# Optimization experiments

Measured on AMD Instinct MI355X. Metric: run time of the kernel, lower is better.

Reference implementation:

```python
import jax, jax.numpy as jnp
import numpy as np

D_MODEL = 1024
NUM_HEADS = 16
HEAD_DIM = D_MODEL // NUM_HEADS
MAX_SEQ_LEN = 2048
THETA = 10000.0
BATCH = 2
SEQ = 2048


def _rope_tables():
    inv_freq = 1.0 / (THETA ** (jnp.arange(0, HEAD_DIM, 2, dtype=jnp.float32) / HEAD_DIM))
    pos = jnp.arange(MAX_SEQ_LEN, dtype=jnp.float32)
    freqs = pos[:, None] * inv_freq[None, :]  # [max_seq, head_dim/2]
    return jnp.sin(freqs), jnp.cos(freqs)


def _apply_rope(x, sin, cos):
    # x: [b, h, s, d]; sin/cos: [s, d/2] -> broadcast over b, h
    sin = sin[None, None, :, :]
    cos = cos[None, None, :, :]
    x_even = x[..., 0::2]
    x_odd = x[..., 1::2]
    out_even = x_even * cos - x_odd * sin
    out_odd = x_even * sin + x_odd * cos
    # interleave back: stack on new last axis then flatten
    out = jnp.stack((out_even, out_odd), axis=-1)
    return out.reshape(x.shape)


def setup_inputs() -> dict:
    key = jax.random.key(0)
    ks = jax.random.split(key, 5)
    std = (2.0 / (D_MODEL + D_MODEL)) ** 0.5
    return {
        "x": jax.random.normal(ks[0], (BATCH, SEQ, D_MODEL), dtype=jnp.float32),
        "Wq": jax.random.normal(ks[1], (D_MODEL, D_MODEL), dtype=jnp.float32) * std,
        "Wk": jax.random.normal(ks[2], (D_MODEL, D_MODEL), dtype=jnp.float32) * std,
        "Wv": jax.random.normal(ks[3], (D_MODEL, D_MODEL), dtype=jnp.float32) * std,
        "Wo": jax.random.normal(ks[4], (D_MODEL, D_MODEL), dtype=jnp.float32) * std,
    }


def reference(x, Wq, Wk, Wv, Wo):
    b, s, _ = x.shape
    # projections: weight stored [out, in] as in the torch Linear
    Q = jnp.einsum('bsd,od->bso', x, Wq)
    K = jnp.einsum('bsd,od->bso', x, Wk)
    V = jnp.einsum('bsd,od->bso', x, Wv)
    # split heads -> [b, h, s, hd]
    def split(t):
        return t.reshape(b, s, NUM_HEADS, HEAD_DIM).transpose(0, 2, 1, 3)
    Q, K, V = split(Q), split(K), split(V)
    sin, cos = _rope_tables()
    sin, cos = sin[:s], cos[:s]
    Q = _apply_rope(Q, sin, cos)
    K = _apply_rope(K, sin, cos)
    scale = 1.0 / jnp.sqrt(jnp.float32(HEAD_DIM))
    scores = jnp.einsum('bhqd,bhkd->bhqk', Q, K)
    causal = jnp.tril(jnp.ones((s, s), dtype=bool))[None, None]
    scores = jnp.where(causal, scores, -jnp.inf) * scale  # -inf * scale stays -inf
    attn = jax.nn.softmax(scores, axis=-1)
    out = jnp.einsum('bhqk,bhkd->bhqd', attn, V)
    out = out.transpose(0, 2, 1, 3).reshape(b, s, D_MODEL)
    return jnp.einsum('bsd,od->bso', out, Wo)
```

## Files before the change

### kernel.cpp

```cpp
#include <hip/hip_runtime.h>
#include <math.h>

#define NHEADS 16
#define HD 64
#define SEQ 2048
#define BATCH 2
#define DM 1024
#define MTOT (BATCH*SEQ)
#define LDP 72

typedef __bf16 bf16x8 __attribute__((ext_vector_type(8)));
typedef __bf16 bf16x4 __attribute__((ext_vector_type(4)));
typedef float  f32x4  __attribute__((ext_vector_type(4)));

#define LOG2E 1.4426950408889634f

#define GLD16(gp, lp) __builtin_amdgcn_global_load_lds( \
    (const __attribute__((address_space(1))) void*)(gp), \
    (__attribute__((address_space(3))) void*)(lp), 16, 0, 0)

__global__ __launch_bounds__(256)
void cast_all(const float* __restrict__ x, const float* __restrict__ Wq,
              const float* __restrict__ Wk, const float* __restrict__ Wv,
              const float* __restrict__ Wo,
              __bf16* __restrict__ xb, __bf16* __restrict__ Wqkvb,
              __bf16* __restrict__ Wob)
{
    const size_t NX = (size_t)MTOT * DM;
    const size_t NW = (size_t)DM * DM;
    const size_t i = ((size_t)blockIdx.x * 256 + threadIdx.x) * 8;
    const float* src; __bf16* dst; size_t off;
    if (i < NX)               { src = x;  dst = xb;           off = i; }
    else if (i < NX + NW)     { src = Wq; dst = Wqkvb;        off = i - NX; }
    else if (i < NX + 2*NW)   { src = Wk; dst = Wqkvb + NW;   off = i - NX - NW; }
    else if (i < NX + 3*NW)   { src = Wv; dst = Wqkvb + 2*NW; off = i - NX - 2*NW; }
    else                      { src = Wo; dst = Wob;          off = i - NX - 3*NW; }
    const float4 f0 = *(const float4*)&src[off];
    const float4 f1 = *(const float4*)&src[off + 4];
    bf16x8 o;
    o[0] = (__bf16)f0.x; o[1] = (__bf16)f0.y; o[2] = (__bf16)f0.z; o[3] = (__bf16)f0.w;
    o[4] = (__bf16)f1.x; o[5] = (__bf16)f1.y; o[6] = (__bf16)f1.z; o[7] = (__bf16)f1.w;
    *(bf16x8*)&dst[off] = o;
}

__global__ __launch_bounds__(256)
void gemm_mfma(const __bf16* __restrict__ A, const __bf16* __restrict__ W,
               float* __restrict__ Cf,
               __bf16* __restrict__ Qb, __bf16* __restrict__ Kb,
               __bf16* __restrict__ Vtb, int mode)
{
    __shared__ __bf16 As[128 * 32];
    __shared__ __bf16 Bs[128 * 32];

    const int tid  = threadIdx.x;
    const int lane = tid & 63;
    const int wave = tid >> 6;
    const int ll   = lane & 15;
    const int quad = lane >> 4;
    const int wm   = (wave & 1) * 64;
    const int wn   = (wave >> 1) * 64;
    const int bm   = blockIdx.x * 128;
    const int bn   = blockIdx.y * 128;

    const __bf16* Ab = A + (size_t)bm * DM;
    const __bf16* Wb = W + (size_t)bn * DM;

    f32x4 acc[4][4];
#pragma unroll
    for (int i = 0; i < 4; i++)
#pragma unroll
        for (int j = 0; j < 4; j++) acc[i][j] = (f32x4){0.f, 0.f, 0.f, 0.f};

    const int t0 = tid, t1 = tid + 256;
    const int ar0 = t0 >> 2, ac0 = (t0 & 3) * 8;
    const int ar1 = t1 >> 2, ac1 = (t1 & 3) * 8;

    for (int k0 = 0; k0 < DM; k0 += 32) {
        GLD16(Ab + (size_t)ar0 * DM + k0 + ac0, &As[t0 * 8]);
        GLD16(Ab + (size_t)ar1 * DM + k0 + ac1, &As[t1 * 8]);
        GLD16(Wb + (size_t)ar0 * DM + k0 + ac0, &Bs[t0 * 8]);
        GLD16(Wb + (size_t)ar1 * DM + k0 + ac1, &Bs[t1 * 8]);
        __syncthreads();

        bf16x8 af[4], bfr[4];
#pragma unroll
        for (int i = 0; i < 4; i++)
            af[i] = *(const bf16x8*)&As[(wm + i*16 + ll) * 32 + quad * 8];
#pragma unroll
        for (int j = 0; j < 4; j++)
            bfr[j] = *(const bf16x8*)&Bs[(wn + j*16 + ll) * 32 + quad * 8];
#pragma unroll
        for (int i = 0; i < 4; i++)
#pragma unroll
            for (int j = 0; j < 4; j++)
                acc[i][j] = __builtin_amdgcn_mfma_f32_16x16x32_bf16(
                    af[i], bfr[j], acc[i][j], 0, 0, 0);

        __syncthreads();
    }

    if (mode == 1) {
#pragma unroll
        for (int i = 0; i < 4; i++) {
#pragma unroll
            for (int j = 0; j < 4; j++) {
                const int gc = bn + wn + j*16 + ll;
#pragma unroll
                for (int r = 0; r < 4; r++) {
                    const int gr = bm + wm + i*16 + quad*4 + r;
                    Cf[(size_t)gr * DM + gc] = acc[i][j][r];
                }
            }
        }
    } else {
        const int which = bn >> 10;
        const int nb = bn & 1023;
#pragma unroll
        for (int i = 0; i < 4; i++) {
            const int m0 = bm + wm + i*16 + quad*4;
            const int b  = m0 >> 11;
            const int s0 = m0 & (SEQ - 1);
#pragma unroll
            for (int j = 0; j < 4; j++) {
                const int n_g = nb + wn + j*16 + ll;
                const int h = n_g >> 6, d = n_g & (HD - 1);
                if (which == 2) {
                    bf16x4 pk;
#pragma unroll
                    for (int r = 0; r < 4; r++) pk[r] = (__bf16)acc[i][j][r];
                    *(bf16x4*)&Vtb[((size_t)((b*NHEADS + h)*HD + d)) * SEQ + s0] = pk;
                } else {
                    __bf16* P = (which == 0) ? Qb : Kb;
#pragma unroll
                    for (int r = 0; r < 4; r++)
                        P[((size_t)(b*NHEADS + h) * SEQ + s0 + r) * HD + d] =
                            (__bf16)acc[i][j][r];
                }
            }
        }
    }
}

__global__ __launch_bounds__(256)
void rope_bf16(__bf16* __restrict__ Q, __bf16* __restrict__ K)
{
    const int t = blockIdx.x * 256 + threadIdx.x;
    __bf16* P = (blockIdx.y == 0) ? Q : K;
    const float sc = (blockIdx.y == 0) ? 0.125f * LOG2E : 1.0f;

    const int d0 = (t & 7) * 8;
    const int s  = (t >> 3) & (SEQ - 1);

    bf16x8 v = *(bf16x8*)&P[(size_t)t * 8];
    bf16x8 o;
#pragma unroll
    for (int k = 0; k < 4; k++) {
        const float inv = exp2f(-(float)(d0 + 2*k) * (13.287712379549449f / 64.0f));
        const float f  = (float)s * inv;
        const float sn = sinf(f);
        const float cs = cosf(f);
        const float xe = (float)v[2*k];
        const float xo = (float)v[2*k + 1];
        o[2*k]     = (__bf16)((xe * cs - xo * sn) * sc);
        o[2*k + 1] = (__bf16)((xe * sn + xo * cs) * sc);
    }
    *(bf16x8*)&P[(size_t)t * 8] = o;
}

__global__ __launch_bounds__(256, 2)
void attn_mfma(const __bf16* __restrict__ Qb, const __bf16* __restrict__ Kb,
               const __bf16* __restrict__ Vtb, __bf16* __restrict__ AOb)
{
    __shared__ __align__(16) __bf16 pt[4][16][LDP];
    __shared__ float comb[4][64][66];
    __shared__ float lbuf[4][64];

    const int tid  = threadIdx.x;
    const int wave = tid >> 6;
    const int lane = tid & 63;
    const int m    = lane & 15;
    const int quad = lane >> 4;
    const int bh   = blockIdx.x;
    const int b    = bh >> 4, h = bh & 15;

    const __bf16* Qp = Qb + (size_t)bh * SEQ * HD;
    const __bf16* Kp = Kb + (size_t)bh * SEQ * HD;
    const __bf16* Vp = Vtb + (size_t)bh * HD * SEQ;

    bf16x8 ones;
#pragma unroll
    for (int j = 0; j < 8; j++) ones[j] = (__bf16)1.0f;

#pragma unroll 1
    for (int pass = 0; pass < 2; pass++) {
        const int qb = pass ? (SEQ/64 - 1) - (int)blockIdx.y : (int)blockIdx.y;
        const int q0 = qb * 64;

        bf16x8 qf[4][2];
#pragma unroll
        for (int i = 0; i < 4; i++) {
            const __bf16* qp = Qp + (size_t)(q0 + i*16 + m) * HD + quad*8;
            qf[i][0] = *(const bf16x8*)qp;
            qf[i][1] = *(const bf16x8*)(qp + 32);
        }

        f32x4 acc[4][4];
        f32x4 l_acc[4];
#pragma unroll
        for (int i = 0; i < 4; i++) {
            l_acc[i] = (f32x4){0.f, 0.f, 0.f, 0.f};
#pragma unroll
            for (int nt = 0; nt < 4; nt++) acc[i][nt] = (f32x4){0.f, 0.f, 0.f, 0.f};
        }

        for (int t = wave; t <= qb; t += 4) {
            const int k0 = t * 64;
            const bool diag = (t == qb);

            bf16x8 kf[4][2], vf[4][2];
#pragma unroll
            for (int tk = 0; tk < 4; tk++) {
                const __bf16* kp = Kp + (size_t)(k0 + tk*16 + m) * HD + quad*8;
                kf[tk][0] = *(const bf16x8*)kp;
                kf[tk][1] = *(const bf16x8*)(kp + 32);
                const __bf16* vp = Vp + (size_t)(tk*16 + m) * SEQ + k0 + quad*8;
                vf[tk][0] = *(const bf16x8*)vp;
                vf[tk][1] = *(const bf16x8*)(vp + 32);
            }

#pragma unroll
            for (int i = 0; i < 4; i++) {
                f32x4 s[4];
#pragma unroll
                for (int tk = 0; tk < 4; tk++) {
                    s[tk] = (f32x4){0.f, 0.f, 0.f, 0.f};
                    s[tk] = __builtin_amdgcn_mfma_f32_16x16x32_bf16(
                        qf[i][0], kf[tk][0], s[tk], 0, 0, 0);
                    s[tk] = __builtin_amdgcn_mfma_f32_16x16x32_bf16(
                        qf[i][1], kf[tk][1], s[tk], 0, 0, 0);
                }
#pragma unroll
                for (int tk = 0; tk < 4; tk++) {
#pragma unroll
                    for (int r = 0; r < 4; r++) {
                        float sv = s[tk][r];
                        if (diag)
                            sv = (16*tk + m <= 16*i + quad*4 + r) ? sv : -INFINITY;
                        const float p = __builtin_amdgcn_exp2f(sv);
                        pt[wave][quad*4 + r][16*tk + m] = (__bf16)p;
                    }
                }
                const bf16x8 af0 = *(const bf16x8*)&pt[wave][m][quad*8];
                const bf16x8 af1 = *(const bf16x8*)&pt[wave][m][32 + quad*8];
                l_acc[i] = __builtin_amdgcn_mfma_f32_16x16x32_bf16(
                    af0, ones, l_acc[i], 0, 0, 0);
                l_acc[i] = __builtin_amdgcn_mfma_f32_16x16x32_bf16(
                    af1, ones, l_acc[i], 0, 0, 0);
#pragma unroll
                for (int nt = 0; nt < 4; nt++) {
                    acc[i][nt] = __builtin_amdgcn_mfma_f32_16x16x32_bf16(
                        af0, vf[nt][0], acc[i][nt], 0, 0, 0);
                    acc[i][nt] = __builtin_amdgcn_mfma_f32_16x16x32_bf16(
                        af1, vf[nt][1], acc[i][nt], 0, 0, 0);
                }
            }
        }

        __syncthreads();
#pragma unroll
        for (int i = 0; i < 4; i++) {
#pragma unroll
            for (int nt = 0; nt < 4; nt++)
#pragma unroll
                for (int r = 0; r < 4; r++)
                    comb[wave][i*16 + quad*4 + r][nt*16 + m] = acc[i][nt][r];
            if (m == 0)
#pragma unroll
                for (int r = 0; r < 4; r++)
                    lbuf[wave][i*16 + quad*4 + r] = l_acc[i][r];
        }
        __syncthreads();

        {
            const int row = tid >> 2;
            const int cg  = (tid & 3) * 16;
            const float l = lbuf[0][row] + lbuf[1][row] + lbuf[2][row] + lbuf[3][row];
            const float rl = 1.0f / l;
            __bf16* op = AOb + (size_t)(b * SEQ + q0 + row) * DM + h * HD + cg;
#pragma unroll
            for (int c = 0; c < 16; c++) {
                const float o = comb[0][row][cg + c] + comb[1][row][cg + c]
                              + comb[2][row][cg + c] + comb[3][row][cg + c];
                op[c] = (__bf16)(o * rl);
            }
        }
        __syncthreads();
    }
}

extern "C" void kernel_launch(void* const* d_in, const int* in_sizes, int n_in,
                              void* d_out, int out_size, void* d_ws, size_t ws_size,
                              hipStream_t stream) {
    const float* x  = (const float*)d_in[0];
    const float* Wq = (const float*)d_in[1];
    const float* Wk = (const float*)d_in[2];
    const float* Wv = (const float*)d_in[3];
    const float* Wo = (const float*)d_in[4];
    float* out = (float*)d_out;

    char* ws = (char*)d_ws;
    __bf16* xb    = (__bf16*)ws;
    __bf16* Wqkvb = (__bf16*)(ws + ((size_t)8  << 20));
    __bf16* Wob   = (__bf16*)(ws + ((size_t)14 << 20));
    __bf16* Qb    = (__bf16*)(ws + ((size_t)16 << 20));
    __bf16* Kb    = (__bf16*)(ws + ((size_t)24 << 20));
    __bf16* Vtb   = (__bf16*)(ws + ((size_t)32 << 20));
    __bf16* AOb   = (__bf16*)(ws + ((size_t)40 << 20));

    cast_all<<<4096, 256, 0, stream>>>(x, Wq, Wk, Wv, Wo, xb, Wqkvb, Wob);

    gemm_mfma<<<dim3(MTOT/128, 3072/128), 256, 0, stream>>>(
        xb, Wqkvb, nullptr, Qb, Kb, Vtb, 0);

    rope_bf16<<<dim3((BATCH*NHEADS*SEQ*8)/256, 2), 256, 0, stream>>>(Qb, Kb);

    attn_mfma<<<dim3(BATCH*NHEADS, SEQ/128), 256, 0, stream>>>(Qb, Kb, Vtb, AOb);

    gemm_mfma<<<dim3(MTOT/128, DM/128), 256, 0, stream>>>(
        AOb, Wob, out, nullptr, nullptr, nullptr, 1);
}
```

Before: 205.7 us.

## Widen GEMM K-tile to 64 with XOR-swizzled LDS and narrower output-projection tiles

The MFMA GEMM now stages a 64-wide K slice per iteration instead of 32, halving the number of barrier pairs. LDS writes and reads use an XOR swizzle on 16-byte groups to avoid bank conflicts. The kernel is templated on the N tile width, and the output projection uses BN=64, doubling its block count for better CU occupancy. This costs more LDS per block and smaller per-wave tiles, with less reuse, for the output GEMM.

```diff
diff --git a/kernel.cpp b/kernel.cpp
--- a/kernel.cpp
+++ b/kernel.cpp
@@ -43,14 +43,16 @@
     *(bf16x8*)&dst[off] = o;
 }
 
+template<int BN>
 __global__ __launch_bounds__(256)
 void gemm_mfma(const __bf16* __restrict__ A, const __bf16* __restrict__ W,
                float* __restrict__ Cf,
                __bf16* __restrict__ Qb, __bf16* __restrict__ Kb,
                __bf16* __restrict__ Vtb, int mode)
 {
-    __shared__ __bf16 As[128 * 32];
-    __shared__ __bf16 Bs[128 * 32];
+    constexpr int JT = BN / 32;
+    __shared__ __bf16 As[128 * 64];
+    __shared__ __bf16 Bs[BN * 64];
 
     const int tid  = threadIdx.x;
     const int lane = tid & 63;
@@ -58,44 +60,56 @@
     const int ll   = lane & 15;
     const int quad = lane >> 4;
     const int wm   = (wave & 1) * 64;
-    const int wn   = (wave >> 1) * 64;
+    const int wn   = (wave >> 1) * (BN / 2);
     const int bm   = blockIdx.x * 128;
-    const int bn   = blockIdx.y * 128;
+    const int bn   = blockIdx.y * BN;
 
     const __bf16* Ab = A + (size_t)bm * DM;
     const __bf16* Wb = W + (size_t)bn * DM;
 
-    f32x4 acc[4][4];
+    f32x4 acc[4][JT];
 #pragma unroll
     for (int i = 0; i < 4; i++)
 #pragma unroll
-        for (int j = 0; j < 4; j++) acc[i][j] = (f32x4){0.f, 0.f, 0.f, 0.f};
-
-    const int t0 = tid, t1 = tid + 256;
-    const int ar0 = t0 >> 2, ac0 = (t0 & 3) * 8;
-    const int ar1 = t1 >> 2, ac1 = (t1 & 3) * 8;
-
-    for (int k0 = 0; k0 < DM; k0 += 32) {
-        GLD16(Ab + (size_t)ar0 * DM + k0 + ac0, &As[t0 * 8]);
-        GLD16(Ab + (size_t)ar1 * DM + k0 + ac1, &As[t1 * 8]);
-        GLD16(Wb + (size_t)ar0 * DM + k0 + ac0, &Bs[t0 * 8]);
-        GLD16(Wb + (size_t)ar1 * DM + k0 + ac1, &Bs[t1 * 8]);
-        __syncthreads();
-
-        bf16x8 af[4], bfr[4];
-#pragma unroll
-        for (int i = 0; i < 4; i++)
-            af[i] = *(const bf16x8*)&As[(wm + i*16 + ll) * 32 + quad * 8];
-#pragma unroll
-        for (int j = 0; j < 4; j++)
-            bfr[j] = *(const bf16x8*)&Bs[(wn + j*16 + ll) * 32 + quad * 8];
-#pragma unroll
-        for (int i = 0; i < 4; i++)
-#pragma unroll
-            for (int j = 0; j < 4; j++)
-                acc[i][j] = __builtin_amdgcn_mfma_f32_16x16x32_bf16(
-                    af[i], bfr[j], acc[i][j], 0, 0, 0);
-
+        for (int j = 0; j < JT; j++) acc[i][j] = (f32x4){0.f, 0.f, 0.f, 0.f};
+
+    for (int k0 = 0; k0 < DM; k0 += 64) {
+#pragma unroll
+        for (int j = 0; j < 4; j++) {
+            const int t = tid + 256 * j;
+            const int r = t >> 3, g = t & 7;
+            GLD16(Ab + (size_t)r * DM + k0 + ((g ^ (r & 7)) * 8), &As[t * 8]);
+        }
+#pragma unroll
+        for (int j = 0; j < BN / 32; j++) {
+            const int t = tid + 256 * j;
+            const int r = t >> 3, g = t & 7;
+            GLD16(Wb + (size_t)r * DM + k0 + ((g ^ (r & 7)) * 8), &Bs[t * 8]);
+        }
+        __syncthreads();
+
+#pragma unroll
+        for (int kh = 0; kh < 2; kh++) {
+            bf16x8 af[4], bfr[JT];
+#pragma unroll
+            for (int i = 0; i < 4; i++) {
+                const int r = wm + i*16 + ll;
+                const int g = kh*4 + quad;
+                af[i] = *(const bf16x8*)&As[(r*8 + (g ^ (r & 7))) * 8];
+            }
+#pragma unroll
+            for (int j = 0; j < JT; j++) {
+                const int r = wn + j*16 + ll;
+                const int g = kh*4 + quad;
+                bfr[j] = *(const bf16x8*)&Bs[(r*8 + (g ^ (r & 7))) * 8];
+            }
+#pragma unroll
+            for (int i = 0; i < 4; i++)
+#pragma unroll
+                for (int j = 0; j < JT; j++)
+                    acc[i][j] = __builtin_amdgcn_mfma_f32_16x16x32_bf16(
+                        af[i], bfr[j], acc[i][j], 0, 0, 0);
+        }
         __syncthreads();
     }
 
@@ -103,7 +117,7 @@
 #pragma unroll
         for (int i = 0; i < 4; i++) {
 #pragma unroll
-            for (int j = 0; j < 4; j++) {
+            for (int j = 0; j < JT; j++) {
                 const int gc = bn + wn + j*16 + ll;
 #pragma unroll
                 for (int r = 0; r < 4; r++) {
@@ -121,7 +135,7 @@
             const int b  = m0 >> 11;
             const int s0 = m0 & (SEQ - 1);
 #pragma unroll
-            for (int j = 0; j < 4; j++) {
+            for (int j = 0; j < JT; j++) {
                 const int n_g = nb + wn + j*16 + ll;
                 const int h = n_g >> 6, d = n_g & (HD - 1);
                 if (which == 2) {
@@ -319,13 +333,13 @@
 
     cast_all<<<4096, 256, 0, stream>>>(x, Wq, Wk, Wv, Wo, xb, Wqkvb, Wob);
 
-    gemm_mfma<<<dim3(MTOT/128, 3072/128), 256, 0, stream>>>(
+    gemm_mfma<128><<<dim3(MTOT/128, 3072/128), 256, 0, stream>>>(
         xb, Wqkvb, nullptr, Qb, Kb, Vtb, 0);
 
     rope_bf16<<<dim3((BATCH*NHEADS*SEQ*8)/256, 2), 256, 0, stream>>>(Qb, Kb);
 
     attn_mfma<<<dim3(BATCH*NHEADS, SEQ/128), 256, 0, stream>>>(Qb, Kb, Vtb, AOb);
 
-    gemm_mfma<<<dim3(MTOT/128, DM/128), 256, 0, stream>>>(
+    gemm_mfma<64><<<dim3(MTOT/128, DM/64), 256, 0, stream>>>(
         AOb, Wob, out, nullptr, nullptr, nullptr, 1);
 }
```

New measurement: 188.3 us. -8.5%, faster.
